# Kernel optimization log

Hardware: AMD Instinct MI355X
Metric: run time of the kernel (lower is better)

The kernel has to match this reference:

```python
import jax, jax.numpy as jnp
import numpy as np


def _bit_reversal_perm(N, num_stages):
    idx = np.arange(N)
    perm = np.zeros(N, dtype=np.int64)
    for _ in range(num_stages):
        perm = (perm << 1) | (idx & 1)
        idx >>= 1
    return perm


def setup_inputs() -> dict:
    key = jax.random.key(0)
    k1, k2 = jax.random.split(key)
    B, N = 4096, 4096
    return {
        "x_re": jax.random.normal(k1, (B, N), dtype=jnp.float32),
        "x_im": jax.random.normal(k2, (B, N), dtype=jnp.float32),
    }


def reference(x_re, x_im):
    # Radix-2 DIT FFT, identical math to HollywoodFFT.forward.
    N = x_re.shape[-1]
    num_stages = int(round(np.log2(N)))
    batch = x_re.shape[:-1]

    # Input permutation is pure wiring: bit-reversal gather.
    perm = jnp.asarray(_bit_reversal_perm(N, num_stages))
    y_re = x_re[..., perm]
    y_im = x_im[..., perm]

    # Twiddle tile: W_N^k = exp(-2*pi*i*k/N) (precomputed constants).
    k = np.arange(N)
    ang = -2.0 * np.pi * k / N
    W_re_all = np.cos(ang).astype(np.float32)
    W_im_all = np.sin(ang).astype(np.float32)

    for s in range(num_stages):  # fixed small loop over log2(N) stages
        stride = 1 << s
        group_size = stride << 1
        # twiddle_idx = j * (N // group_size) for j in [0, stride), same for every group
        tw = np.arange(stride) * (N // group_size)
        W_re = jnp.asarray(W_re_all[tw])  # (stride,)
        W_im = jnp.asarray(W_im_all[tw])

        # (..., N) -> (..., N//group_size, 2, stride): [...,g,0,j]=upper, [...,g,1,j]=lower
        yr = y_re.reshape(*batch, N // group_size, 2, stride)
        yi = y_im.reshape(*batch, N // group_size, 2, stride)
        a_re, b_re = yr[..., 0, :], yr[..., 1, :]
        a_im, b_im = yi[..., 0, :], yi[..., 1, :]

        wb_re = W_re * b_re - W_im * b_im
        wb_im = W_re * b_im + W_im * b_re

        y_re = jnp.stack([a_re + wb_re, a_re - wb_re], axis=-2).reshape(*batch, N)
        y_im = jnp.stack([a_im + wb_im, a_im - wb_im], axis=-2).reshape(*batch, N)

    return y_re, y_im
```

## Files before the change

kernel.cpp:

```cpp
#include <hip/hip_runtime.h>


#define NFFT 4096

typedef float fvec4 __attribute__((ext_vector_type(4)));

__device__ __forceinline__ void fft16(float xr[16], float xi[16]) {
    const int br[16] = {0,8,4,12,2,10,6,14,1,9,5,13,3,11,7,15};
    float yr[16], yi[16];
#pragma unroll
    for (int j = 0; j < 16; ++j) { yr[j] = xr[br[j]]; yi[j] = xi[br[j]]; }
    const float W16r[8] = { 1.0f,  0.92387953251128675613f,  0.70710678118654752440f,
                            0.38268343236508977173f,  0.0f, -0.38268343236508977173f,
                           -0.70710678118654752440f, -0.92387953251128675613f };
    const float W16i[8] = { 0.0f, -0.38268343236508977173f, -0.70710678118654752440f,
                           -0.92387953251128675613f, -1.0f, -0.92387953251128675613f,
                           -0.70710678118654752440f, -0.38268343236508977173f };
#pragma unroll
    for (int s = 0; s < 4; ++s) {
        const int stride = 1 << s;
        const int tm = 8 >> s;
#pragma unroll
        for (int g = 0; g < 16; g += 2 * stride) {
#pragma unroll
            for (int p = 0; p < stride; ++p) {
                const int i0 = g + p, i1 = i0 + stride;
                const float twr = W16r[p * tm], twi = W16i[p * tm];
                const float brr = yr[i1] * twr - yi[i1] * twi;
                const float bii = yr[i1] * twi + yi[i1] * twr;
                const float ar = yr[i0], ai = yi[i0];
                yr[i0] = ar + brr; yi[i0] = ai + bii;
                yr[i1] = ar - brr; yi[i1] = ai - bii;
            }
        }
    }
#pragma unroll
    for (int j = 0; j < 16; ++j) { xr[j] = yr[j]; xi[j] = yi[j]; }
}

__global__ __launch_bounds__(256, 5)
void HollywoodFFT_53584011985637_kernel(const float* __restrict__ xre,
                                        const float* __restrict__ xim,
                                        float* __restrict__ outre,
                                        float* __restrict__ outim) {
    __shared__ __align__(16) float lr[NFFT];
    __shared__ __align__(16) float li[NFFT];

    const int t = threadIdx.x;
    const long long row = blockIdx.x;
    const float* __restrict__ xr_row = xre + row * NFFT;
    const float* __restrict__ xi_row = xim + row * NFFT;

    {
        const fvec4* __restrict__ xr4 = (const fvec4*)xr_row;
        const fvec4* __restrict__ xi4 = (const fvec4*)xi_row;
        fvec4 rr[4], ii[4];
#pragma unroll
        for (int q = 0; q < 4; ++q) { rr[q] = xr4[t + 256 * q]; ii[q] = xi4[t + 256 * q]; }
#pragma unroll
        for (int q = 0; q < 4; ++q) {
            ((fvec4*)lr)[t + 256 * q] = rr[q];
            ((fvec4*)li)[t + 256 * q] = ii[q];
        }
    }
    __syncthreads();

    float vr[16], vi[16];
    const int a = t & 15;
    const int u = t >> 4;

#pragma unroll
    for (int c = 0; c < 16; ++c) { vr[c] = lr[t + 256 * c]; vi[c] = li[t + 256 * c]; }
    fft16(vr, vi);
    __syncthreads();
#pragma unroll
    for (int uu = 0; uu < 16; ++uu) {
        const int id = a + 16 * ((t >> 4) ^ uu) + 256 * uu;
        lr[id] = vr[uu]; li[id] = vi[uu];
    }
    __syncthreads();

    {
        float s0, c0;
        __sincosf(-6.28318530717958647692f * (float)u * (1.0f / 256.0f), &s0, &c0);
        float twr = 1.0f, twi = 0.0f;
#pragma unroll
        for (int bb = 0; bb < 16; ++bb) {
            const int id = a + 16 * (bb ^ u) + 256 * u;
            const float rr = lr[id], ii = li[id];
            vr[bb] = rr * twr - ii * twi;
            vi[bb] = rr * twi + ii * twr;
            const float ntr = twr * c0 - twi * s0;
            twi = twr * s0 + twi * c0;
            twr = ntr;
        }
    }
    fft16(vr, vi);
    __syncthreads();
#pragma unroll
    for (int v = 0; v < 16; ++v) {
        const int id = (a ^ u) + 16 * (u ^ v) + 256 * v;
        lr[id] = vr[v]; li[id] = vi[v];
    }
    __syncthreads();

    const int u2 = t & 15, v2 = t >> 4;
    {
        float s0, c0;
        __sincosf(-6.28318530717958647692f * (float)(u2 + 16 * v2) * (1.0f / 4096.0f),
                  &s0, &c0);
        float twr = 1.0f, twi = 0.0f;
#pragma unroll
        for (int aa = 0; aa < 16; ++aa) {
            const int id = (aa ^ u2) + 16 * (u2 ^ v2) + 256 * v2;
            const float rr = lr[id], ii = li[id];
            vr[aa] = rr * twr - ii * twi;
            vi[aa] = rr * twi + ii * twr;
            const float ntr = twr * c0 - twi * s0;
            twi = twr * s0 + twi * c0;
            twr = ntr;
        }
    }
    fft16(vr, vi);
    __syncthreads();
#pragma unroll
    for (int w = 0; w < 16; ++w) {
        const int id = u2 + 16 * v2 + 256 * w;
        lr[id] = vr[w]; li[id] = vi[w];
    }
    __syncthreads();

    {
        float* __restrict__ or_row = outre + row * NFFT;
        float* __restrict__ oi_row = outim + row * NFFT;
#pragma unroll
        for (int q = 0; q < 4; ++q) {
            fvec4 rr = ((const fvec4*)lr)[t + 256 * q];
            fvec4 ii = ((const fvec4*)li)[t + 256 * q];
            __builtin_nontemporal_store(rr, (fvec4*)or_row + t + 256 * q);
            __builtin_nontemporal_store(ii, (fvec4*)oi_row + t + 256 * q);
        }
    }
}

extern "C" void kernel_launch(void* const* d_in, const int* in_sizes, int n_in,
                              void* d_out, int out_size, void* d_ws, size_t ws_size,
                              hipStream_t stream) {
    const float* xre = (const float*)d_in[0];
    const float* xim = (const float*)d_in[1];
    const int B = in_sizes[0] / NFFT;
    float* out = (float*)d_out;
    float* outre = out;
    float* outim = out + (size_t)B * NFFT;
    HollywoodFFT_53584011985637_kernel<<<dim3(B), dim3(256), 0, stream>>>(
        xre, xim, outre, outim);
}
```

Baseline: 235.4 us.

## Load/store global directly in FFT passes, interleave LDS complex pairs, cut barriers

Removes the LDS staging of input and output: the first radix-16 pass reads strided scalars straight from global memory, and the last pass writes results directly with non-temporal scalar stores. The shared buffer becomes interleaved float2 so each LDS access moves a complex pair. The second-to-third pass transpose is rewritten with rotated indexing and a restarted twiddle recurrence, which removes several barriers. The trade-off is that global accesses become scalar rather than 16-byte vectors (still coalesced across threads), and the rotated twiddle logic adds extra select work.

New measurement: 236.9 us. No clear change (+0.6%).

```diff
diff --git a/kernel.cpp b/kernel.cpp
--- a/kernel.cpp
+++ b/kernel.cpp
@@ -2,8 +2,6 @@
 
 
 #define NFFT 4096
-
-typedef float fvec4 __attribute__((ext_vector_type(4)));
 
 __device__ __forceinline__ void fft16(float xr[16], float xi[16]) {
     const int br[16] = {0,8,4,12,2,10,6,14,1,9,5,13,3,11,7,15};
@@ -43,103 +41,78 @@
                                         const float* __restrict__ xim,
                                         float* __restrict__ outre,
                                         float* __restrict__ outim) {
-    __shared__ __align__(16) float lr[NFFT];
-    __shared__ __align__(16) float li[NFFT];
+    __shared__ __align__(16) float2 l[NFFT];
 
     const int t = threadIdx.x;
     const long long row = blockIdx.x;
     const float* __restrict__ xr_row = xre + row * NFFT;
     const float* __restrict__ xi_row = xim + row * NFFT;
 
-    {
-        const fvec4* __restrict__ xr4 = (const fvec4*)xr_row;
-        const fvec4* __restrict__ xi4 = (const fvec4*)xi_row;
-        fvec4 rr[4], ii[4];
-#pragma unroll
-        for (int q = 0; q < 4; ++q) { rr[q] = xr4[t + 256 * q]; ii[q] = xi4[t + 256 * q]; }
-#pragma unroll
-        for (int q = 0; q < 4; ++q) {
-            ((fvec4*)lr)[t + 256 * q] = rr[q];
-            ((fvec4*)li)[t + 256 * q] = ii[q];
-        }
-    }
-    __syncthreads();
-
     float vr[16], vi[16];
     const int a = t & 15;
-    const int u = t >> 4;
+    const int h = t >> 4;
 
 #pragma unroll
-    for (int c = 0; c < 16; ++c) { vr[c] = lr[t + 256 * c]; vi[c] = li[t + 256 * c]; }
+    for (int c = 0; c < 16; ++c) {
+        vr[c] = xr_row[t + 256 * c];
+        vi[c] = xi_row[t + 256 * c];
+    }
     fft16(vr, vi);
-    __syncthreads();
 #pragma unroll
     for (int uu = 0; uu < 16; ++uu) {
-        const int id = a + 16 * ((t >> 4) ^ uu) + 256 * uu;
-        lr[id] = vr[uu]; li[id] = vi[uu];
+        l[a + 16 * (h ^ uu) + 256 * uu] = make_float2(vr[uu], vi[uu]);
     }
     __syncthreads();
 
     {
         float s0, c0;
-        __sincosf(-6.28318530717958647692f * (float)u * (1.0f / 256.0f), &s0, &c0);
+        __sincosf(-6.28318530717958647692f * (float)h * (1.0f / 256.0f), &s0, &c0);
         float twr = 1.0f, twi = 0.0f;
 #pragma unroll
         for (int bb = 0; bb < 16; ++bb) {
-            const int id = a + 16 * (bb ^ u) + 256 * u;
-            const float rr = lr[id], ii = li[id];
-            vr[bb] = rr * twr - ii * twi;
-            vi[bb] = rr * twi + ii * twr;
+            const float2 xv = l[a + 16 * (bb ^ h) + 256 * h];
+            vr[bb] = xv.x * twr - xv.y * twi;
+            vi[bb] = xv.x * twi + xv.y * twr;
             const float ntr = twr * c0 - twi * s0;
             twi = twr * s0 + twi * c0;
             twr = ntr;
         }
     }
     fft16(vr, vi);
-    __syncthreads();
 #pragma unroll
     for (int v = 0; v < 16; ++v) {
-        const int id = (a ^ u) + 16 * (u ^ v) + 256 * v;
-        lr[id] = vr[v]; li[id] = vi[v];
+        l[a + 16 * v + 256 * h] = make_float2(vr[v], vi[v]);
     }
     __syncthreads();
 
-    const int u2 = t & 15, v2 = t >> 4;
+    const int u2 = a, v2 = h;
     {
-        float s0, c0;
-        __sincosf(-6.28318530717958647692f * (float)(u2 + 16 * v2) * (1.0f / 4096.0f),
-                  &s0, &c0);
-        float twr = 1.0f, twi = 0.0f;
+        const int K = u2 + 16 * v2;
+        float sW, cW;
+        __sincosf(-6.28318530717958647692f * (float)K * (1.0f / 4096.0f), &sW, &cW);
+        const int m0 = (u2 * K) & 4095;
+        float twr, twi;
+        __sincosf(-6.28318530717958647692f * (float)m0 * (1.0f / 4096.0f), &twi, &twr);
 #pragma unroll
-        for (int aa = 0; aa < 16; ++aa) {
-            const int id = (aa ^ u2) + 16 * (u2 ^ v2) + 256 * v2;
-            const float rr = lr[id], ii = li[id];
-            vr[aa] = rr * twr - ii * twi;
-            vi[aa] = rr * twi + ii * twr;
-            const float ntr = twr * c0 - twi * s0;
-            twi = twr * s0 + twi * c0;
-            twr = ntr;
+        for (int s = 0; s < 16; ++s) {
+            const int aa = (s + u2) & 15;
+            const float2 xv = l[aa + 16 * v2 + 256 * u2];
+            vr[aa] = xv.x * twr - xv.y * twi;
+            vi[aa] = xv.x * twi + xv.y * twr;
+            const float ntr = twr * cW - twi * sW;
+            const float nti = twr * sW + twi * cW;
+            twr = (aa == 15) ? 1.0f : ntr;
+            twi = (aa == 15) ? 0.0f : nti;
         }
     }
     fft16(vr, vi);
-    __syncthreads();
+
+    float* __restrict__ or_row = outre + row * NFFT;
+    float* __restrict__ oi_row = outim + row * NFFT;
 #pragma unroll
     for (int w = 0; w < 16; ++w) {
-        const int id = u2 + 16 * v2 + 256 * w;
-        lr[id] = vr[w]; li[id] = vi[w];
-    }
-    __syncthreads();
-
-    {
-        float* __restrict__ or_row = outre + row * NFFT;
-        float* __restrict__ oi_row = outim + row * NFFT;
-#pragma unroll
-        for (int q = 0; q < 4; ++q) {
-            fvec4 rr = ((const fvec4*)lr)[t + 256 * q];
-            fvec4 ii = ((const fvec4*)li)[t + 256 * q];
-            __builtin_nontemporal_store(rr, (fvec4*)or_row + t + 256 * q);
-            __builtin_nontemporal_store(ii, (fvec4*)oi_row + t + 256 * q);
-        }
+        __builtin_nontemporal_store(vr[w], or_row + t + 256 * w);
+        __builtin_nontemporal_store(vi[w], oi_row + t + 256 * w);
     }
 }
 
```
